# Kernel optimization log

Hardware: AMD Instinct MI355X
Metric: run time of the kernel (lower is better)

Reference implementation:

```python
import jax, jax.numpy as jnp
import numpy as np

NUM_TOKENS = 16384
HIDDEN = 4096
NUM_EXPERTS = 256
TOP_K = 8
N_GROUP = 8
TOPK_GROUP = 4
NORM_TOPK_PROB = True
ROUTED_SCALING_FACTOR = 1.0


def setup_inputs() -> dict:
    key = jax.random.key(0)
    k1, k2, k3 = jax.random.split(key, 3)
    hidden_states = jax.random.normal(k1, (NUM_TOKENS, HIDDEN), dtype=jnp.float32)
    weight = jax.random.normal(k2, (NUM_EXPERTS, HIDDEN), dtype=jnp.float32) * (HIDDEN ** -0.5)
    e_score_correction_bias = jax.random.normal(k3, (NUM_EXPERTS,), dtype=jnp.float32) * 0.01
    return {"hidden_states": hidden_states, "weight": weight,
            "e_score_correction_bias": e_score_correction_bias}


def reference(hidden_states, weight, e_score_correction_bias):
    num_tokens = hidden_states.shape[0]
    # router logits: [T, E]
    logits = jnp.einsum('th,eh->te', hidden_states.astype(jnp.float32),
                        weight.astype(jnp.float32))
    scores = jax.nn.sigmoid(logits)
    scores_for_choice = scores + e_score_correction_bias[None, :]
    # group scores: sum of top-2 within each group, [T, G]
    per_group = scores_for_choice.reshape(num_tokens, N_GROUP, NUM_EXPERTS // N_GROUP)
    top2_vals, _ = jax.lax.top_k(per_group, 2)
    group_scores = top2_vals.sum(axis=-1)
    # select topk_group groups, build mask over experts
    _, group_idx = jax.lax.top_k(group_scores, TOPK_GROUP)  # [T, topk_group]
    group_mask = jnp.zeros_like(group_scores).at[
        jnp.arange(num_tokens)[:, None], group_idx].set(1.0)  # [T, G]
    score_mask = jnp.repeat(group_mask, NUM_EXPERTS // N_GROUP, axis=1)  # [T, E]
    tmp_scores = jnp.where(score_mask > 0, scores_for_choice, -jnp.inf)
    # final top-k experts over masked scores
    _, topk_idx = jax.lax.top_k(tmp_scores, TOP_K)  # [T, K]
    topk_weight = jnp.take_along_axis(scores, topk_idx, axis=1)
    if TOP_K > 1 and NORM_TOPK_PROB:
        denom = topk_weight.sum(axis=-1, keepdims=True) + 1e-20
        topk_weight = topk_weight / denom
    topk_weight = topk_weight * ROUTED_SCALING_FACTOR
    return logits, topk_weight, topk_idx
```

## Files before the change

### kernel.cpp

```cpp
#include <hip/hip_runtime.h>
#include <hip/hip_bf16.h>
#include <math.h>

#define TKN 16384
#define HID 4096
#define NE  256
#define TOPK 8
#define NGRP 8
#define TOPG 4

#define BM 128
#define BN 64
#define BK 64
#define NKT (HID / BK)
#define BIMG 16384

typedef _Float16 half8 __attribute__((ext_vector_type(8)));
typedef float    f32x4 __attribute__((ext_vector_type(4)));

static __device__ __forceinline__ unsigned pkrtz(float x, float y) {
    auto r = __builtin_amdgcn_cvt_pkrtz(x, y);
    return __builtin_bit_cast(unsigned, r);
}
static __device__ __forceinline__ float hi_mask(float a) {
    return __uint_as_float(__float_as_uint(a) & 0xFFFFE000u);
}

__global__ __launch_bounds__(256) void prep_b(const float* __restrict__ B,
                                              unsigned char* __restrict__ ws)
{
    const int gid = blockIdx.x * 256 + threadIdx.x;
    const int e   = gid >> 9;
    const int k0  = (gid & 511) * 8;
    const float* src = B + (size_t)e * HID + k0;
    float v[8];
    #pragma unroll
    for (int i = 0; i < 8; ++i) v[i] = src[i];
    unsigned hw[4], lw[4];
    #pragma unroll
    for (int j = 0; j < 4; ++j) {
        const float x0 = v[2*j], x1 = v[2*j+1];
        const float h0 = hi_mask(x0), h1 = hi_mask(x1);
        hw[j] = pkrtz(h0, h1);
        lw[j] = pkrtz(x0 - h0, x1 - h1);
    }
    const int cb     = e >> 6;
    const int colgrp = (e & 63) >> 4;
    const int lane16 = e & 15;
    const int kt     = k0 >> 6;
    const int kk     = k0 & 63;
    const int wg     = kk >> 5;
    const int kseg   = (kk >> 3) & 3;
    const int f      = colgrp * 2 + wg;
    unsigned char* img = ws + (size_t)(cb * NKT + kt) * BIMG
                            + f * 2048 + (kseg * 16 + lane16) * 16;
    *(uint4*)(img)        = make_uint4(hw[0], hw[1], hw[2], hw[3]);
    *(uint4*)(img + 1024) = make_uint4(lw[0], lw[1], lw[2], lw[3]);
}

__global__ __launch_bounds__(512, 4) void gemm_mfma(
    const float* __restrict__ A, const unsigned char* __restrict__ Bws,
    float* __restrict__ C)
{
    __shared__ __align__(16) unsigned char smem[2][2][16384];

    const int tid  = threadIdx.x;
    const int lane = tid & 63;
    const int wave = tid >> 6;
    const int wg = wave >> 2;
    const int wr = (wave >> 1) & 1;
    const int wc = wave & 1;

    const int logical = (blockIdx.x & 7) * 64 + (blockIdx.x >> 3);
    const int mb   = logical >> 2;
    const int cb   = logical & 3;
    const int row0 = mb * BM;

    const int arow = tid >> 2;
    const int aseg = (tid & 3) * 16;
    const float* aG = A + (size_t)(row0 + arow) * HID + aseg;
    const int xorw = (arow & 7) << 4;
    const int awx0 = arow * 128 + ((aseg * 2) ^ xorw);
    const int awx1 = arow * 128 + ((aseg * 2 + 16) ^ xorw);

    const int kx    = ((wg * 64) + ((lane >> 4) << 4)) ^ ((lane & 7) << 4);
    const int aRowB = (wr * 64 + (lane & 15)) * 128;

    const unsigned char* bBase = Bws + (size_t)cb * NKT * BIMG;
    const int f0off = ((wc * 2 + 0) * 2 + wg) * 2048 + lane * 16;
    const int f1off = ((wc * 2 + 1) * 2 + wg) * 2048 + lane * 16;

    f32x4 acc[4][2];
    #pragma unroll
    for (int i = 0; i < 4; ++i) { acc[i][0] = (f32x4)0.f; acc[i][1] = (f32x4)0.f; }

    float4 av[4];
    half8 bC[4], bN[4];

    #pragma unroll
    for (int i = 0; i < 4; ++i) av[i] = *(const float4*)(aG + i * 4);
    bC[0] = *(const half8*)(bBase + f0off);
    bC[1] = *(const half8*)(bBase + f0off + 1024);
    bC[2] = *(const half8*)(bBase + f1off);
    bC[3] = *(const half8*)(bBase + f1off + 1024);
    {
        unsigned hw[8], lw[8];
        const float f[16] = {av[0].x,av[0].y,av[0].z,av[0].w, av[1].x,av[1].y,av[1].z,av[1].w,
                             av[2].x,av[2].y,av[2].z,av[2].w, av[3].x,av[3].y,av[3].z,av[3].w};
        #pragma unroll
        for (int j = 0; j < 8; ++j) {
            const float h0 = hi_mask(f[2*j]), h1 = hi_mask(f[2*j+1]);
            hw[j] = pkrtz(h0, h1);
            lw[j] = pkrtz(f[2*j] - h0, f[2*j+1] - h1);
        }
        *(uint4*)&smem[0][0][awx0] = make_uint4(hw[0], hw[1], hw[2], hw[3]);
        *(uint4*)&smem[0][0][awx1] = make_uint4(hw[4], hw[5], hw[6], hw[7]);
        *(uint4*)&smem[0][1][awx0] = make_uint4(lw[0], lw[1], lw[2], lw[3]);
        *(uint4*)&smem[0][1][awx1] = make_uint4(lw[4], lw[5], lw[6], lw[7]);
    }
    __syncthreads();

#define GSTEP(KT, BCUR, BNXT)                                                  \
    {                                                                          \
        const int kt_ = (KT);                                                  \
        const unsigned char* ub = &smem[kt_ & 1][0][0];                        \
        const bool more = (kt_ != NKT - 1);                                    \
        if (more) {                    \
            const float* ap = aG + (kt_ + 1) * BK;                             \
            av[0] = *(const float4*)(ap);                                      \
            av[1] = *(const float4*)(ap + 4);                                  \
            av[2] = *(const float4*)(ap + 8);                                  \
            av[3] = *(const float4*)(ap + 12);                                 \
            const unsigned char* bp = bBase + (size_t)(kt_ + 1) * BIMG;        \
            BNXT[0] = *(const half8*)(bp + f0off);                             \
            BNXT[1] = *(const half8*)(bp + f0off + 1024);                      \
            BNXT[2] = *(const half8*)(bp + f1off);                             \
            BNXT[3] = *(const half8*)(bp + f1off + 1024);                      \
        }                                                                      \
        __builtin_amdgcn_sched_barrier(0);                                     \
        _Pragma("unroll")                                                      \
        for (int mt = 0; mt < 4; ++mt) {                                       \
            const half8 ah = *(const half8*)(ub + aRowB + mt * 2048 + kx);     \
            const half8 al = *(const half8*)(ub + 16384 + aRowB + mt * 2048 + kx); \
            f32x4 c0 = acc[mt][0];                                             \
            c0 = __builtin_amdgcn_mfma_f32_16x16x32_f16(ah, BCUR[0], c0, 0, 0, 0); \
            c0 = __builtin_amdgcn_mfma_f32_16x16x32_f16(ah, BCUR[1], c0, 0, 0, 0); \
            c0 = __builtin_amdgcn_mfma_f32_16x16x32_f16(al, BCUR[0], c0, 0, 0, 0); \
            acc[mt][0] = c0;                                                   \
            f32x4 c1 = acc[mt][1];                                             \
            c1 = __builtin_amdgcn_mfma_f32_16x16x32_f16(ah, BCUR[2], c1, 0, 0, 0); \
            c1 = __builtin_amdgcn_mfma_f32_16x16x32_f16(ah, BCUR[3], c1, 0, 0, 0); \
            c1 = __builtin_amdgcn_mfma_f32_16x16x32_f16(al, BCUR[2], c1, 0, 0, 0); \
            acc[mt][1] = c1;                                                   \
        }                                                                      \
        if (more) {        \
            const int nb = (kt_ + 1) & 1;                                      \
            unsigned hw[8], lw[8];                                             \
            const float f[16] = {av[0].x,av[0].y,av[0].z,av[0].w,              \
                                 av[1].x,av[1].y,av[1].z,av[1].w,              \
                                 av[2].x,av[2].y,av[2].z,av[2].w,              \
                                 av[3].x,av[3].y,av[3].z,av[3].w};             \
            _Pragma("unroll")                                                  \
            for (int j = 0; j < 8; ++j) {                                      \
                const float h0 = hi_mask(f[2*j]), h1 = hi_mask(f[2*j+1]);      \
                hw[j] = pkrtz(h0, h1);                                         \
                lw[j] = pkrtz(f[2*j] - h0, f[2*j+1] - h1);                     \
            }                                                                  \
            *(uint4*)&smem[nb][0][awx0] = make_uint4(hw[0], hw[1], hw[2], hw[3]); \
            *(uint4*)&smem[nb][0][awx1] = make_uint4(hw[4], hw[5], hw[6], hw[7]); \
            *(uint4*)&smem[nb][1][awx0] = make_uint4(lw[0], lw[1], lw[2], lw[3]); \
            *(uint4*)&smem[nb][1][awx1] = make_uint4(lw[4], lw[5], lw[6], lw[7]); \
        }                                                                      \
        __syncthreads();                                                       \
    }

    for (int kt = 0; kt < NKT; kt += 2) {
        GSTEP(kt,     bC, bN);
        GSTEP(kt + 1, bN, bC);
    }
#undef GSTEP

    float* redf = (float*)&smem[0][0][0];
    const int fb = (wave & 3) * 2048 + lane * 4;
    if (wg == 1) {
        #pragma unroll
        for (int mt = 0; mt < 4; ++mt)
            #pragma unroll
            for (int nt = 0; nt < 2; ++nt)
                *(f32x4*)&redf[fb + (mt * 2 + nt) * 256] = acc[mt][nt];
    }
    __syncthreads();
    if (wg == 0) {
        #pragma unroll
        for (int mt = 0; mt < 4; ++mt) {
            #pragma unroll
            for (int nt = 0; nt < 2; ++nt) {
                f32x4 o = acc[mt][nt] + *(const f32x4*)&redf[fb + (mt * 2 + nt) * 256];
                const int r0 = row0 + wr * 64 + mt * 16 + (lane >> 4) * 4;
                const int cc = cb * BN + wc * 32 + nt * 16 + (lane & 15);
                #pragma unroll
                for (int r = 0; r < 4; ++r)
                    C[(size_t)(r0 + r) * NE + cc] = o[r];
            }
        }
    }
}

__global__ __launch_bounds__(256) void router_topk_kernel(
    const float* __restrict__ logits, const float* __restrict__ bias,
    float* __restrict__ out_w, float* __restrict__ out_i)
{
    const int wid  = threadIdx.x >> 6;
    const int lane = threadIdx.x & 63;
    const int token = blockIdx.x * 4 + wid;

    const float* row = logits + (size_t)token * NE;
    const float4 lg = *(const float4*)&row[lane * 4];

    float sig[4], sc[4];
    {
        const float l4[4] = {lg.x, lg.y, lg.z, lg.w};
        #pragma unroll
        for (int j = 0; j < 4; ++j) {
            sig[j] = 1.f / (1.f + expf(-l4[j]));
            sc[j]  = sig[j] + bias[lane * 4 + j];
        }
    }

    float m1 = sc[0], m2 = -INFINITY;
    #pragma unroll
    for (int j = 1; j < 4; ++j) {
        if (sc[j] > m1) { m2 = m1; m1 = sc[j]; }
        else if (sc[j] > m2) { m2 = sc[j]; }
    }
    #pragma unroll
    for (int off = 1; off < 8; off <<= 1) {
        const float o1 = __shfl_xor(m1, off);
        const float o2 = __shfl_xor(m2, off);
        const float lo = fminf(m1, o1);
        m1 = fmaxf(m1, o1);
        m2 = fmaxf(lo, fmaxf(m2, o2));
    }
    const float gscore = m1 + m2;

    const int gmy = lane >> 3;
    int rank = 0;
    #pragma unroll
    for (int g = 0; g < NGRP; ++g) {
        const float gs = __shfl(gscore, g * 8);
        if (gs > gscore || (gs == gscore && g < gmy)) ++rank;
    }
    if (rank >= TOPG) {
        #pragma unroll
        for (int j = 0; j < 4; ++j) sc[j] = -INFINITY;
    }

    float wk[TOPK]; int ik[TOPK];
    float wsum = 0.f;
    #pragma unroll
    for (int k = 0; k < TOPK; ++k) {
        float bv = sc[0]; int bi = lane * 4;
        #pragma unroll
        for (int j = 1; j < 4; ++j)
            if (sc[j] > bv) { bv = sc[j]; bi = lane * 4 + j; }
        #pragma unroll
        for (int off = 1; off < 64; off <<= 1) {
            const float v2 = __shfl_xor(bv, off);
            const int   i2 = __shfl_xor(bi, off);
            if (v2 > bv || (v2 == bv && i2 < bi)) { bv = v2; bi = i2; }
        }
        const int owner = bi >> 2;
        const int j = bi & 3;
        const float sv = (j == 0) ? sig[0] : (j == 1) ? sig[1] : (j == 2) ? sig[2] : sig[3];
        const float w = __shfl(sv, owner);
        wk[k] = w; ik[k] = bi; wsum += w;
        if (lane == owner) {
            if (j == 0) sc[0] = -INFINITY;
            else if (j == 1) sc[1] = -INFINITY;
            else if (j == 2) sc[2] = -INFINITY;
            else sc[3] = -INFINITY;
        }
    }

    if (lane == 0) {
        const float denom = wsum + 1e-20f;
        #pragma unroll
        for (int k = 0; k < TOPK; ++k) {
            out_w[(size_t)token * TOPK + k] = wk[k] / denom;
            out_i[(size_t)token * TOPK + k] = (float)ik[k];
        }
    }
}

extern "C" void kernel_launch(void* const* d_in, const int* in_sizes, int n_in,
                              void* d_out, int out_size, void* d_ws, size_t ws_size,
                              hipStream_t stream) {
    const float* hidden = (const float*)d_in[0];
    const float* weight = (const float*)d_in[1];
    const float* bias   = (const float*)d_in[2];

    float* logits = (float*)d_out;
    float* out_w  = logits + (size_t)TKN * NE;
    float* out_i  = out_w + (size_t)TKN * TOPK;

    unsigned char* bpl = (unsigned char*)d_ws;

    prep_b<<<512, 256, 0, stream>>>(weight, bpl);
    gemm_mfma<<<512, 512, 0, stream>>>(hidden, bpl, logits);
    router_topk_kernel<<<TKN / 4, 256, 0, stream>>>(logits, bias, out_w, out_i);
}
```

Measured before the change: 171.8 us.

## Stream raw fp32 A tiles via global_load_lds and split to fp16 at MFMA time

The GEMM now copies fp32 A tiles straight from global memory into LDS with global_load_lds, using an XOR-swizzled layout, instead of staging them through registers and splitting them into hi/lo fp16 halves before storing. The hi/lo split now happens after the LDS read, just before the MFMAs. The block tile shrinks to 64 rows with 256 threads and 1024 blocks, and LDS use halves. This removes register staging and the conversion from the load path. In exchange, every wave redoes the split work for each fragment it reads, and the smaller M tile lowers reuse of the B fragments.

```diff
diff --git a/kernel.cpp b/kernel.cpp
--- a/kernel.cpp
+++ b/kernel.cpp
@@ -9,8 +9,7 @@
 #define NGRP 8
 #define TOPG 4
 
-#define BM 128
-#define BN 64
+#define BM 64
 #define BK 64
 #define NKT (HID / BK)
 #define BIMG 16384
@@ -24,6 +23,11 @@
 }
 static __device__ __forceinline__ float hi_mask(float a) {
     return __uint_as_float(__float_as_uint(a) & 0xFFFFE000u);
+}
+static __device__ __forceinline__ void gload_lds16(const void* g, void* l) {
+    __builtin_amdgcn_global_load_lds(
+        (const __attribute__((address_space(1))) unsigned int*)g,
+        (__attribute__((address_space(3))) unsigned int*)l, 16, 0, 0);
 }
 
 __global__ __launch_bounds__(256) void prep_b(const float* __restrict__ B,
@@ -58,33 +62,36 @@
     *(uint4*)(img + 1024) = make_uint4(lw[0], lw[1], lw[2], lw[3]);
 }
 
-__global__ __launch_bounds__(512, 4) void gemm_mfma(
+__global__ __launch_bounds__(256, 4) void gemm_mfma(
     const float* __restrict__ A, const unsigned char* __restrict__ Bws,
     float* __restrict__ C)
 {
-    __shared__ __align__(16) unsigned char smem[2][2][16384];
+    __shared__ __align__(16) unsigned char smem[2][16384];
 
     const int tid  = threadIdx.x;
     const int lane = tid & 63;
     const int wave = tid >> 6;
-    const int wg = wave >> 2;
-    const int wr = (wave >> 1) & 1;
+    const int wg = wave >> 1;
     const int wc = wave & 1;
 
-    const int logical = (blockIdx.x & 7) * 64 + (blockIdx.x >> 3);
+    const int logical = (blockIdx.x & 7) * 128 + (blockIdx.x >> 3);
     const int mb   = logical >> 2;
     const int cb   = logical & 3;
     const int row0 = mb * BM;
 
-    const int arow = tid >> 2;
-    const int aseg = (tid & 3) * 16;
-    const float* aG = A + (size_t)(row0 + arow) * HID + aseg;
-    const int xorw = (arow & 7) << 4;
-    const int awx0 = arow * 128 + ((aseg * 2) ^ xorw);
-    const int awx1 = arow * 128 + ((aseg * 2 + 16) ^ xorw);
-
-    const int kx    = ((wg * 64) + ((lane >> 4) << 4)) ^ ((lane & 7) << 4);
-    const int aRowB = (wr * 64 + (lane & 15)) * 128;
+    const unsigned char* Abytes = (const unsigned char*)A;
+    const unsigned char* srcp[4];
+    #pragma unroll
+    for (int i = 0; i < 4; ++i) {
+        const int row = 16 * wave + 4 * i + (lane >> 4);
+        srcp[i] = Abytes + (size_t)(row0 + row) * (HID * 4)
+                         + (((lane & 15) * 16) ^ ((row & 7) << 4));
+    }
+    const int ldsW = wave * 4096;
+
+    const int laneA0 = (lane & 15) * 256 +
+                       ((wg * 128 + (lane >> 4) * 32) ^ ((lane & 7) << 4));
+    const int laneA1 = laneA0 ^ 16;
 
     const unsigned char* bBase = Bws + (size_t)cb * NKT * BIMG;
     const int f0off = ((wc * 2 + 0) * 2 + wg) * 2048 + lane * 16;
@@ -94,43 +101,28 @@
     #pragma unroll
     for (int i = 0; i < 4; ++i) { acc[i][0] = (f32x4)0.f; acc[i][1] = (f32x4)0.f; }
 
-    float4 av[4];
     half8 bC[4], bN[4];
 
     #pragma unroll
-    for (int i = 0; i < 4; ++i) av[i] = *(const float4*)(aG + i * 4);
+    for (int i = 0; i < 4; ++i)
+        gload_lds16(srcp[i], &smem[0][ldsW + i * 1024]);
     bC[0] = *(const half8*)(bBase + f0off);
     bC[1] = *(const half8*)(bBase + f0off + 1024);
     bC[2] = *(const half8*)(bBase + f1off);
     bC[3] = *(const half8*)(bBase + f1off + 1024);
-    {
-        unsigned hw[8], lw[8];
-        const float f[16] = {av[0].x,av[0].y,av[0].z,av[0].w, av[1].x,av[1].y,av[1].z,av[1].w,
-                             av[2].x,av[2].y,av[2].z,av[2].w, av[3].x,av[3].y,av[3].z,av[3].w};
-        #pragma unroll
-        for (int j = 0; j < 8; ++j) {
-            const float h0 = hi_mask(f[2*j]), h1 = hi_mask(f[2*j+1]);
-            hw[j] = pkrtz(h0, h1);
-            lw[j] = pkrtz(f[2*j] - h0, f[2*j+1] - h1);
-        }
-        *(uint4*)&smem[0][0][awx0] = make_uint4(hw[0], hw[1], hw[2], hw[3]);
-        *(uint4*)&smem[0][0][awx1] = make_uint4(hw[4], hw[5], hw[6], hw[7]);
-        *(uint4*)&smem[0][1][awx0] = make_uint4(lw[0], lw[1], lw[2], lw[3]);
-        *(uint4*)&smem[0][1][awx1] = make_uint4(lw[4], lw[5], lw[6], lw[7]);
-    }
     __syncthreads();
 
 #define GSTEP(KT, BCUR, BNXT)                                                  \
     {                                                                          \
         const int kt_ = (KT);                                                  \
-        const unsigned char* ub = &smem[kt_ & 1][0][0];                        \
+        const unsigned char* ub = &smem[kt_ & 1][0];                           \
         const bool more = (kt_ != NKT - 1);                                    \
-        if (more) {                    \
-            const float* ap = aG + (kt_ + 1) * BK;                             \
-            av[0] = *(const float4*)(ap);                                      \
-            av[1] = *(const float4*)(ap + 4);                                  \
-            av[2] = *(const float4*)(ap + 8);                                  \
-            av[3] = *(const float4*)(ap + 12);                                 \
+        if (more) {         \
+            unsigned char* nb = &smem[(kt_ + 1) & 1][0];                       \
+            _Pragma("unroll")                                                  \
+            for (int i = 0; i < 4; ++i)                                        \
+                gload_lds16(srcp[i] + (size_t)(kt_ + 1) * 256,                 \
+                            nb + ldsW + i * 1024);                             \
             const unsigned char* bp = bBase + (size_t)(kt_ + 1) * BIMG;        \
             BNXT[0] = *(const half8*)(bp + f0off);                             \
             BNXT[1] = *(const half8*)(bp + f0off + 1024);                      \
@@ -140,8 +132,23 @@
         __builtin_amdgcn_sched_barrier(0);                                     \
         _Pragma("unroll")                                                      \
         for (int mt = 0; mt < 4; ++mt) {                                       \
-            const half8 ah = *(const half8*)(ub + aRowB + mt * 2048 + kx);     \
-            const half8 al = *(const half8*)(ub + 16384 + aRowB + mt * 2048 + kx); \
+            const float4 u0 = *(const float4*)(ub + laneA0 + mt * 4096);       \
+            const float4 u1 = *(const float4*)(ub + laneA1 + mt * 4096);       \
+            const float h0 = hi_mask(u0.x), h1 = hi_mask(u0.y),                \
+                        h2 = hi_mask(u0.z), h3 = hi_mask(u0.w);                \
+            const float h4 = hi_mask(u1.x), h5 = hi_mask(u1.y),                \
+                        h6 = hi_mask(u1.z), h7 = hi_mask(u1.w);                \
+            unsigned ahw[4], alw[4];                                           \
+            ahw[0] = pkrtz(h0, h1);            ahw[1] = pkrtz(h2, h3);         \
+            ahw[2] = pkrtz(h4, h5);            ahw[3] = pkrtz(h6, h7);         \
+            alw[0] = pkrtz(u0.x - h0, u0.y - h1);                              \
+            alw[1] = pkrtz(u0.z - h2, u0.w - h3);                              \
+            alw[2] = pkrtz(u1.x - h4, u1.y - h5);                              \
+            alw[3] = pkrtz(u1.z - h6, u1.w - h7);                              \
+            const half8 ah = __builtin_bit_cast(half8,                         \
+                make_uint4(ahw[0], ahw[1], ahw[2], ahw[3]));                   \
+            const half8 al = __builtin_bit_cast(half8,                         \
+                make_uint4(alw[0], alw[1], alw[2], alw[3]));                   \
             f32x4 c0 = acc[mt][0];                                             \
             c0 = __builtin_amdgcn_mfma_f32_16x16x32_f16(ah, BCUR[0], c0, 0, 0, 0); \
             c0 = __builtin_amdgcn_mfma_f32_16x16x32_f16(ah, BCUR[1], c0, 0, 0, 0); \
@@ -153,24 +160,6 @@
             c1 = __builtin_amdgcn_mfma_f32_16x16x32_f16(al, BCUR[2], c1, 0, 0, 0); \
             acc[mt][1] = c1;                                                   \
         }                                                                      \
-        if (more) {        \
-            const int nb = (kt_ + 1) & 1;                                      \
-            unsigned hw[8], lw[8];                                             \
-            const float f[16] = {av[0].x,av[0].y,av[0].z,av[0].w,              \
-                                 av[1].x,av[1].y,av[1].z,av[1].w,              \
-                                 av[2].x,av[2].y,av[2].z,av[2].w,              \
-                                 av[3].x,av[3].y,av[3].z,av[3].w};             \
-            _Pragma("unroll")                                                  \
-            for (int j = 0; j < 8; ++j) {                                      \
-                const float h0 = hi_mask(f[2*j]), h1 = hi_mask(f[2*j+1]);      \
-                hw[j] = pkrtz(h0, h1);                                         \
-                lw[j] = pkrtz(f[2*j] - h0, f[2*j+1] - h1);                     \
-            }                                                                  \
-            *(uint4*)&smem[nb][0][awx0] = make_uint4(hw[0], hw[1], hw[2], hw[3]); \
-            *(uint4*)&smem[nb][0][awx1] = make_uint4(hw[4], hw[5], hw[6], hw[7]); \
-            *(uint4*)&smem[nb][1][awx0] = make_uint4(lw[0], lw[1], lw[2], lw[3]); \
-            *(uint4*)&smem[nb][1][awx1] = make_uint4(lw[4], lw[5], lw[6], lw[7]); \
-        }                                                                      \
         __syncthreads();                                                       \
     }
 
@@ -180,8 +169,8 @@
     }
 #undef GSTEP
 
-    float* redf = (float*)&smem[0][0][0];
-    const int fb = (wave & 3) * 2048 + lane * 4;
+    float* redf = (float*)&smem[0][0];
+    const int fb = wc * 2048 + lane * 4;
     if (wg == 1) {
         #pragma unroll
         for (int mt = 0; mt < 4; ++mt)
@@ -196,8 +185,8 @@
             #pragma unroll
             for (int nt = 0; nt < 2; ++nt) {
                 f32x4 o = acc[mt][nt] + *(const f32x4*)&redf[fb + (mt * 2 + nt) * 256];
-                const int r0 = row0 + wr * 64 + mt * 16 + (lane >> 4) * 4;
-                const int cc = cb * BN + wc * 32 + nt * 16 + (lane & 15);
+                const int r0 = row0 + mt * 16 + (lane >> 4) * 4;
+                const int cc = cb * 64 + wc * 32 + nt * 16 + (lane & 15);
                 #pragma unroll
                 for (int r = 0; r < 4; ++r)
                     C[(size_t)(r0 + r) * NE + cc] = o[r];
@@ -306,6 +295,6 @@
     unsigned char* bpl = (unsigned char*)d_ws;
 
     prep_b<<<512, 256, 0, stream>>>(weight, bpl);
-    gemm_mfma<<<512, 512, 0, stream>>>(hidden, bpl, logits);
+    gemm_mfma<<<1024, 256, 0, stream>>>(hidden, bpl, logits);
     router_topk_kernel<<<TKN / 4, 256, 0, stream>>>(logits, bias, out_w, out_i);
 }
```

Result: no change. 172.8 us (+0.6%).
